# Performance work log

Hardware: AMD Instinct MI355X
Metric: run time of the kernel (lower is better)

Reference implementation:

```python
import jax, jax.numpy as jnp
import numpy as np

N = 131072
N_SIGMAS = 64
SEG = N // N_SIGMAS  # 2048, also the gaussian window size


def setup_inputs() -> dict:
    key = jax.random.key(0)
    ks = jax.random.split(key, 4)
    n, h = 256, 256
    x = jax.random.normal(ks[0], (n,), dtype=jnp.float32)
    W1 = jax.random.normal(ks[1], (n, h), dtype=jnp.float32) / jnp.sqrt(jnp.float32(n))
    b1 = jnp.zeros((h,), dtype=jnp.float32)
    W2 = jax.random.normal(ks[2], (h, N_SIGMAS), dtype=jnp.float32) / jnp.sqrt(jnp.float32(h))
    b2 = jnp.zeros((N_SIGMAS,), dtype=jnp.float32)
    W3 = jax.random.normal(ks[3], (n, N), dtype=jnp.float32) / jnp.sqrt(jnp.float32(n))
    b3 = jnp.zeros((N,), dtype=jnp.float32)
    return {"x": x, "W1": W1, "b1": b1, "W2": W2, "b2": b2, "W3": W3, "b3": b3}


def _gaussian_windows(sigmas):
    # gaussian_kernel(window_size=SEG, sigma) vmapped over sigmas -> (n_sigmas, SEG)
    mu = SEG / 2.0
    t = jnp.arange(SEG, dtype=sigmas.dtype)
    w = jnp.exp(-((t[None, :] - mu) ** 2) / (2.0 * sigmas[:, None] ** 2))
    return w / jnp.sum(w, axis=1, keepdims=True)


def reference(x, W1, b1, W2, b2, W3, b3):
    # sigma-predictor MLP: Dense -> swish -> Dense
    s = jax.nn.swish(jnp.dot(x, W1) + b1)
    sigmas = jnp.dot(s, W2) + b2              # (n_sigmas,)
    y = jnp.dot(x, W3) + b3                   # (N,)
    windows = _gaussian_windows(sigmas)       # (n_sigmas, SEG)
    segs = y.reshape(N_SIGMAS, SEG)           # equal split, N divisible by n_sigmas
    out = jax.vmap(lambda a, w: jnp.convolve(a, w, mode="same"))(segs, windows)
    return out.reshape(-1)                    # hstack of segments
```

## Files before the change

kernel.cpp:

```cpp
#include <hip/hip_runtime.h>
#include <math.h>

#define NTOT 131072
#define NSIG 64
#define SEGL 2048
#define NIN 256


__global__ __launch_bounds__(256) void k_y(
    const float* __restrict__ x,  const float* __restrict__ W1,
    const float* __restrict__ b1, const float* __restrict__ W2,
    const float* __restrict__ b2, const float* __restrict__ W3,
    const float* __restrict__ b3, float* __restrict__ y,
    float* __restrict__ w_all, int* __restrict__ Dv)
{
  __shared__ float xl[NIN];
  __shared__ float sl[256];
  __shared__ float red[4];
  __shared__ float bc[2];

  const int t = threadIdx.x;
  const int bx0 = (int)blockIdx.x;
  const int bx = ((bx0 & 7) << 5) | (bx0 >> 3);
  const int col = (bx << 9) + (t << 1);

  xl[t] = x[t];
  __syncthreads();

  const float* p = W3 + col;
  const float2 bv = *reinterpret_cast<const float2*>(b3 + col);
  float a0 = bv.x, a1 = bv.y;

  if (bx0 < NSIG) {
    float am = b1[t];
    #pragma unroll 16
    for (int n = 0; n < NIN; ++n) {
      const float xv = xl[n];
      const float2 wv = *reinterpret_cast<const float2*>(p + (size_t)n * NTOT);
      a0 = fmaf(xv, wv.x, a0);
      a1 = fmaf(xv, wv.y, a1);
      am = fmaf(xv, W1[n * 256 + t], am);
    }
    *reinterpret_cast<float2*>(y + col) = make_float2(a0, a1);
    sl[t] = am / (1.0f + expf(-am));
    __syncthreads();

    const int seg = bx0;
    float v = sl[t] * W2[t * NSIG + seg];
    #pragma unroll
    for (int o = 32; o > 0; o >>= 1) v += __shfl_down(v, o, 64);
    const int lane = t & 63, wid = t >> 6;
    if (lane == 0) red[wid] = v;
    __syncthreads();
    if (t == 0) bc[0] = red[0] + red[1] + red[2] + red[3] + b2[seg];
    __syncthreads();
    const float sig = bc[0];

    const float inv2 = 1.0f / (2.0f * sig * sig);
    const float Df = 12.0f * fabsf(sig) + 4.0f;
    const int D = (Df >= 1024.0f) ? 1024 : (int)Df;
    const int dlo = -D;
    const int dhi = (D < 1023) ? D : 1023;
    const int cnt = dhi - dlo + 1;

    float zp = 0.0f;
    for (int i = t; i < cnt; i += 256) {
      const float d = (float)(dlo + i);
      const float e = expf(-d * d * inv2);
      w_all[seg * SEGL + 1024 + dlo + i] = e;
      zp += e;
    }
    v = zp;
    #pragma unroll
    for (int o = 32; o > 0; o >>= 1) v += __shfl_down(v, o, 64);
    if (lane == 0) red[wid] = v;
    __syncthreads();
    if (t == 0) bc[1] = red[0] + red[1] + red[2] + red[3];
    __syncthreads();
    const float iZ = 1.0f / bc[1];
    for (int i = t; i < cnt; i += 256)
      w_all[seg * SEGL + 1024 + dlo + i] *= iZ;
    if (t == 0) Dv[seg] = D;
  } else {
    #pragma unroll 16
    for (int n = 0; n < NIN; ++n) {
      const float xv = xl[n];
      const float2 wv = *reinterpret_cast<const float2*>(p + (size_t)n * NTOT);
      a0 = fmaf(xv, wv.x, a0);
      a1 = fmaf(xv, wv.y, a1);
    }
    *reinterpret_cast<float2*>(y + col) = make_float2(a0, a1);
  }
}

__global__ __launch_bounds__(256) void k_conv(
    const float* __restrict__ y, const float* __restrict__ w_all,
    const int* __restrict__ Dv, float* __restrict__ out)
{
  __shared__ float S[2560];

  const int t = threadIdx.x;
  const int bx0 = (int)blockIdx.x;
  const int bx = ((bx0 & 7) << 6) | (bx0 >> 3);
  const int seg = bx >> 3;
  const int M0 = (bx & 7) << 8;
  const int sbase = M0 - 1026;

  const int D = Dv[seg];
  const int dlo = -D;
  const int dhi = (D < 1023) ? D : 1023;

  const int ilo = 1025 - dhi;
  const int ihi = 1281 + D;
  for (int i = ilo + t; i < ihi; i += 256) {
    const int g = sbase + i;
    S[i] = (g >= 0 && g < SEGL) ? y[seg * SEGL + g] : 0.0f;
  }
  __syncthreads();

  const float* wrow = w_all + seg * SEGL + 1024;
  float a = 0.0f;
  for (int d = dlo; d <= dhi; ++d)
    a = fmaf(wrow[d], S[t + 1025 - d], a);
  out[seg * SEGL + M0 + t] = a;
}

extern "C" void kernel_launch(void* const* d_in, const int* in_sizes, int n_in,
                              void* d_out, int out_size, void* d_ws, size_t ws_size,
                              hipStream_t stream) {
  const float* x  = (const float*)d_in[0];
  const float* W1 = (const float*)d_in[1];
  const float* b1 = (const float*)d_in[2];
  const float* W2 = (const float*)d_in[3];
  const float* b2 = (const float*)d_in[4];
  const float* W3 = (const float*)d_in[5];
  const float* b3 = (const float*)d_in[6];
  float* out = (float*)d_out;

  char* ws = (char*)d_ws;
  float* y     = (float*)(ws);
  float* w_all = (float*)(ws + 524288);
  int*   Dv    = (int*)  (ws + 1048576);

  hipLaunchKernelGGL(k_y, dim3(256), dim3(256), 0, stream,
                     x, W1, b1, W2, b2, W3, b3, y, w_all, Dv);
  hipLaunchKernelGGL(k_conv, dim3(512), dim3(256), 0, stream,
                     y, w_all, Dv, out);
}
```

Before: 36.23 us.

## Split GEMV reduction dimension across two thread halves and double grid size

The y = x·W3 GEMV now uses 512 blocks of 256 columns each, with the 256-long input dimension split between two groups of 128 threads. The partial sums are combined through shared memory. The sigma MLP is computed only after the W3 work, in its own separate loop. This gives more blocks in flight on a 256-CU device to hide memory latency while streaming the 128 MB W3 matrix. The cost is an extra shared-memory reduction and a barrier.

```diff
diff --git a/kernel.cpp b/kernel.cpp
--- a/kernel.cpp
+++ b/kernel.cpp
@@ -15,82 +15,86 @@
     float* __restrict__ w_all, int* __restrict__ Dv)
 {
   __shared__ float xl[NIN];
+  __shared__ float2 part[256];
   __shared__ float sl[256];
   __shared__ float red[4];
   __shared__ float bc[2];
 
   const int t = threadIdx.x;
   const int bx0 = (int)blockIdx.x;
-  const int bx = ((bx0 & 7) << 5) | (bx0 >> 3);
-  const int col = (bx << 9) + (t << 1);
+  const int bx = ((bx0 & 7) << 6) | (bx0 >> 3);
+  const int colbase = bx << 8;
+  const int g = t >> 7;
+  const int p = t & 127;
+  const int c = colbase + (p << 1);
 
   xl[t] = x[t];
   __syncthreads();
 
-  const float* p = W3 + col;
-  const float2 bv = *reinterpret_cast<const float2*>(b3 + col);
-  float a0 = bv.x, a1 = bv.y;
+  const float* wp = W3 + (size_t)(g << 7) * NTOT + c;
+  float a0 = 0.0f, a1 = 0.0f;
+  #pragma unroll 16
+  for (int k = 0; k < 128; ++k) {
+    const float xv = xl[(g << 7) + k];
+    const float2 wv = *reinterpret_cast<const float2*>(wp + (size_t)k * NTOT);
+    a0 = fmaf(xv, wv.x, a0);
+    a1 = fmaf(xv, wv.y, a1);
+  }
+  part[t] = make_float2(a0, a1);
+  __syncthreads();
 
-  if (bx0 < NSIG) {
-    float am = b1[t];
-    #pragma unroll 16
-    for (int n = 0; n < NIN; ++n) {
-      const float xv = xl[n];
-      const float2 wv = *reinterpret_cast<const float2*>(p + (size_t)n * NTOT);
-      a0 = fmaf(xv, wv.x, a0);
-      a1 = fmaf(xv, wv.y, a1);
-      am = fmaf(xv, W1[n * 256 + t], am);
-    }
-    *reinterpret_cast<float2*>(y + col) = make_float2(a0, a1);
-    sl[t] = am / (1.0f + expf(-am));
-    __syncthreads();
+  if (t < 128) {
+    const float2 q0 = part[t];
+    const float2 q1 = part[t + 128];
+    const float2 bv = *reinterpret_cast<const float2*>(b3 + colbase + (t << 1));
+    *reinterpret_cast<float2*>(y + colbase + (t << 1)) =
+        make_float2(q0.x + q1.x + bv.x, q0.y + q1.y + bv.y);
+  }
 
-    const int seg = bx0;
-    float v = sl[t] * W2[t * NSIG + seg];
-    #pragma unroll
-    for (int o = 32; o > 0; o >>= 1) v += __shfl_down(v, o, 64);
-    const int lane = t & 63, wid = t >> 6;
-    if (lane == 0) red[wid] = v;
-    __syncthreads();
-    if (t == 0) bc[0] = red[0] + red[1] + red[2] + red[3] + b2[seg];
-    __syncthreads();
-    const float sig = bc[0];
+  if (bx0 >= NSIG) return;
 
-    const float inv2 = 1.0f / (2.0f * sig * sig);
-    const float Df = 12.0f * fabsf(sig) + 4.0f;
-    const int D = (Df >= 1024.0f) ? 1024 : (int)Df;
-    const int dlo = -D;
-    const int dhi = (D < 1023) ? D : 1023;
-    const int cnt = dhi - dlo + 1;
+  float am = b1[t];
+  #pragma unroll 32
+  for (int n = 0; n < NIN; ++n) am = fmaf(xl[n], W1[n * 256 + t], am);
+  sl[t] = am / (1.0f + expf(-am));
+  __syncthreads();
 
-    float zp = 0.0f;
-    for (int i = t; i < cnt; i += 256) {
-      const float d = (float)(dlo + i);
-      const float e = expf(-d * d * inv2);
-      w_all[seg * SEGL + 1024 + dlo + i] = e;
-      zp += e;
-    }
-    v = zp;
-    #pragma unroll
-    for (int o = 32; o > 0; o >>= 1) v += __shfl_down(v, o, 64);
-    if (lane == 0) red[wid] = v;
-    __syncthreads();
-    if (t == 0) bc[1] = red[0] + red[1] + red[2] + red[3];
-    __syncthreads();
-    const float iZ = 1.0f / bc[1];
-    for (int i = t; i < cnt; i += 256)
-      w_all[seg * SEGL + 1024 + dlo + i] *= iZ;
-    if (t == 0) Dv[seg] = D;
-  } else {
-    #pragma unroll 16
-    for (int n = 0; n < NIN; ++n) {
-      const float xv = xl[n];
-      const float2 wv = *reinterpret_cast<const float2*>(p + (size_t)n * NTOT);
-      a0 = fmaf(xv, wv.x, a0);
-      a1 = fmaf(xv, wv.y, a1);
-    }
-    *reinterpret_cast<float2*>(y + col) = make_float2(a0, a1);
+  const int seg = bx0;
+  float v = sl[t] * W2[t * NSIG + seg];
+  #pragma unroll
+  for (int o = 32; o > 0; o >>= 1) v += __shfl_down(v, o, 64);
+  const int lane = t & 63, wid = t >> 6;
+  if (lane == 0) red[wid] = v;
+  __syncthreads();
+  if (t == 0) bc[0] = red[0] + red[1] + red[2] + red[3] + b2[seg];
+  __syncthreads();
+  const float sig = bc[0];
+
+  const float inv2 = 1.0f / (2.0f * sig * sig);
+  const float Df = 12.0f * fabsf(sig) + 4.0f;
+  const int D = (Df >= 1024.0f) ? 1024 : (int)Df;
+  const int dlo = -D;
+  const int dhi = (D < 1023) ? D : 1023;
+  const int cnt = dhi - dlo + 1;
+
+  float zp = 0.0f;
+  for (int i = t; i < cnt; i += 256) {
+    const float d = (float)(dlo + i);
+    const float e = expf(-d * d * inv2);
+    w_all[seg * SEGL + 1024 + dlo + i] = e;
+    zp += e;
   }
+  v = zp;
+  #pragma unroll
+  for (int o = 32; o > 0; o >>= 1) v += __shfl_down(v, o, 64);
+  if (lane == 0) red[wid] = v;
+  __syncthreads();
+  if (t == 0) bc[1] = red[0] + red[1] + red[2] + red[3];
+  __syncthreads();
+  const float iZ = 1.0f / bc[1];
+  for (int i = t; i < cnt; i += 256)
+    w_all[seg * SEGL + 1024 + dlo + i] *= iZ;
+  if (t == 0) Dv[seg] = D;
 }
 
 __global__ __launch_bounds__(256) void k_conv(
@@ -142,7 +146,7 @@
   float* w_all = (float*)(ws + 524288);
   int*   Dv    = (int*)  (ws + 1048576);
 
-  hipLaunchKernelGGL(k_y, dim3(256), dim3(256), 0, stream,
+  hipLaunchKernelGGL(k_y, dim3(512), dim3(256), 0, stream,
                      x, W1, b1, W2, b2, W3, b3, y, w_all, Dv);
   hipLaunchKernelGGL(k_conv, dim3(512), dim3(256), 0, stream,
                      y, w_all, Dv, out);
```

Measured after the change: 32.88 us. 9.2% less time.
